# Kernel optimization log

Measured on AMD Instinct MI355X. Metric: run time of the kernel, lower is better.

## Reference

```python
import jax, jax.numpy as jnp
import numpy as np

N = 100000
E = 1600000
D_IN = 128
H = 128
C = 3
EPS_BN = 1e-5
EPS_LN = 1e-5


def _gcn_conv(x, W, b, src, dst, ew, n):
    # PyG GCNConv: x' = D^{-1/2} (A + I) D^{-1/2} (x W) + b, self-loop weight 1
    x = x @ W
    loop = jnp.arange(n)
    src2 = jnp.concatenate([src, loop])
    dst2 = jnp.concatenate([dst, loop])
    ew2 = jnp.concatenate([ew, jnp.ones((n,), dtype=x.dtype)])
    deg = jax.ops.segment_sum(ew2, dst2, num_segments=n)
    dinv = jnp.where(deg > 0, jax.lax.rsqrt(jnp.maximum(deg, 1e-12)), 0.0)
    norm = dinv[src2] * ew2 * dinv[dst2]  # [E+N]
    msgs = x[src2] * norm[:, None]        # [E+N, H] gathered messages
    out = jax.ops.segment_sum(msgs, dst2, num_segments=n)
    return out + b


def setup_inputs() -> dict:
    key = jax.random.key(0)
    ks = jax.random.split(key, 16)
    def lin(k, i, o):
        s = 1.0 / np.sqrt(i)
        k1, k2 = jax.random.split(k)
        return (jax.random.uniform(k1, (i, o), jnp.float32, -s, s),
                jax.random.uniform(k2, (o,), jnp.float32, -s, s))
    x = jax.random.normal(ks[0], (N, D_IN), jnp.float32)
    edge_index = jax.random.randint(ks[1], (2, E), 0, N, jnp.int64)
    edge_attr = jax.random.uniform(ks[2], (E, 1), jnp.float32)
    W_pre, b_pre = lin(ks[3], D_IN, H)
    W1, b1 = lin(ks[4], H, H)
    W2, b2 = lin(ks[5], H, H)
    Wc1, bc1 = lin(ks[6], H, H)
    Wc2, bc2 = lin(ks[7], H, C)
    return {
        "x": x, "edge_index": edge_index, "edge_attr": edge_attr,
        "W_pre": W_pre, "b_pre": b_pre,
        "bn_gamma": jnp.ones((H,), jnp.float32), "bn_beta": jnp.zeros((H,), jnp.float32),
        "bn_mean": jnp.zeros((H,), jnp.float32), "bn_var": jnp.ones((H,), jnp.float32),
        "W1": W1, "b1": b1, "W2": W2, "b2": b2,
        "Wc1": Wc1, "bc1": bc1,
        "ln_g": jnp.ones((H,), jnp.float32), "ln_b": jnp.zeros((H,), jnp.float32),
        "Wc2": Wc2, "bc2": bc2,
    }


def reference(x, edge_index, edge_attr, W_pre, b_pre, bn_gamma, bn_beta, bn_mean, bn_var,
              W1, b1, W2, b2, Wc1, bc1, ln_g, ln_b, Wc2, bc2):
    src, dst = edge_index[0], edge_index[1]
    ew = edge_attr.squeeze()
    n = x.shape[0]
    # input_preprocess: Linear -> BatchNorm1d (eval: running stats) -> ReLU (dropout=identity)
    h = x @ W_pre + b_pre
    h = (h - bn_mean) * jax.lax.rsqrt(bn_var + EPS_BN) * bn_gamma + bn_beta
    h = jax.nn.relu(h)
    residual = h
    # conv layer 1 (+ ReLU, dropout identity in eval)
    h = jax.nn.relu(_gcn_conv(h, W1, b1, src, dst, ew, n))
    # conv layer 2 (last: no activation)
    h = _gcn_conv(h, W2, b2, src, dst, ew, n)
    h = h + residual  # shapes match
    # classifier: Linear -> LayerNorm -> ReLU -> (dropout) -> Linear
    z = h @ Wc1 + bc1
    mu = jnp.mean(z, axis=-1, keepdims=True)
    var = jnp.mean((z - mu) ** 2, axis=-1, keepdims=True)
    z = (z - mu) * jax.lax.rsqrt(var + EPS_LN) * ln_g + ln_b
    z = jax.nn.relu(z)
    return z @ Wc2 + bc2
```

## Files before the change

kernel.cpp:

```cpp
#include <hip/hip_runtime.h>
#include <hip/hip_bf16.h>

typedef __bf16 bf16_t;
typedef bf16_t bf16x8 __attribute__((ext_vector_type(8)));
typedef bf16_t bf16x4 __attribute__((ext_vector_type(4)));
typedef float f32x4 __attribute__((ext_vector_type(4)));
typedef float f32x2 __attribute__((ext_vector_type(2)));

#define EPS_BN 1e-5f
#define EPS_LN 1e-5f
#define SLOTS 32
#define WSCALE 32767.f
#define WINV (1.f / 32767.f)
#define RNODES 448
#define OV_CAP 16384
#define OVA_CAP 65536

__device__ __forceinline__ float blo(unsigned u) { return __uint_as_float(u << 16); }
__device__ __forceinline__ float bhi(unsigned u) { return __uint_as_float(u & 0xFFFF0000u); }
__device__ __forceinline__ f32x2 f8lo(unsigned u) { return __builtin_amdgcn_cvt_pk_f32_fp8((int)u, false); }
__device__ __forceinline__ f32x2 f8hi(unsigned u) { return __builtin_amdgcn_cvt_pk_f32_fp8((int)u, true); }


__global__ void prepK(const float* __restrict__ W0, const float* __restrict__ W1,
                      const float* __restrict__ W2, const float* __restrict__ W3,
                      bf16_t* __restrict__ WT, int* __restrict__ bCnt,
                      int* __restrict__ ovCnt, int* __restrict__ ovACnt) {
    int flat = blockIdx.x * 256 + threadIdx.x;
    if (flat == 0) { *ovCnt = 0; *ovACnt = 0; }
    if (flat < 4096) bCnt[flat] = 0;
    if (flat < 65536) {
        int which = flat >> 14, r = flat & 16383;
        const float* W = (which == 0) ? W0 : (which == 1) ? W1 : (which == 2) ? W2 : W3;
        int i = r >> 7, o = r & 127;
        WT[which * 128 * 136 + o * 136 + i] = (bf16_t)W[r];
    }
}


__global__ __launch_bounds__(256) void binK(
    const int* __restrict__ ei, const float* __restrict__ ea,
    uint2* __restrict__ bbuf, int* __restrict__ bCnt,
    uint2* __restrict__ ovA, int* __restrict__ ovACnt,
    int E, int cap, int nbuck)
{
    __shared__ int lcnt[256];
    __shared__ int gbase[256];
    int tid = threadIdx.x;
    if (tid < nbuck) lcnt[tid] = 0;
    __syncthreads();

    int e0 = blockIdx.x * 4096 + tid;
    int d[16]; unsigned pk[16]; int p[16];
#pragma unroll
    for (int k = 0; k < 16; ++k) {
        int e = e0 + k * 256;
        p[k] = -1;
        if (e < E) {
            d[k] = ei[E + e];
            int s = ei[e];
            unsigned wq = __float2uint_rn(ea[e] * WSCALE);
            pk[k] = ((unsigned)s << 15) | wq;
            p[k] = atomicAdd(&lcnt[(unsigned)d[k] / RNODES], 1);
        }
    }
    __syncthreads();
    if (tid < nbuck) gbase[tid] = atomicAdd(&bCnt[tid * 16], lcnt[tid]);
    __syncthreads();
#pragma unroll
    for (int k = 0; k < 16; ++k) {
        if (p[k] >= 0) {
            int b = (unsigned)d[k] / RNODES;
            int idx = gbase[b] + p[k];
            if (idx < cap) {
                bbuf[(size_t)b * cap + idx] = make_uint2((unsigned)d[k], pk[k]);
            } else {
                int o = atomicAdd(ovACnt, 1);
                if (o < OVA_CAP) ovA[o] = make_uint2((unsigned)d[k], pk[k]);
            }
        }
    }
}


__global__ __launch_bounds__(256) void buildK(
    const uint2* __restrict__ bbuf, const int* __restrict__ bCnt,
    const uint2* __restrict__ ovA, const int* __restrict__ ovACnt,
    unsigned* __restrict__ slots, int* __restrict__ cnt, float* __restrict__ dinv,
    uint2* __restrict__ ov, int* __restrict__ ovCnt,
    int cap, int n)
{
    __shared__ unsigned slotsL[RNODES * 32];
    __shared__ int cntL[RNODES];
    __shared__ float wsumL[RNODES];
    int tid = threadIdx.x;
    int base = blockIdx.x * RNODES;

    for (int j = tid; j < RNODES; j += 256) { cntL[j] = 0; wsumL[j] = 0.f; }
    __syncthreads();

    int nb = min(bCnt[blockIdx.x * 16], cap);
    const uint2* buf = bbuf + (size_t)blockIdx.x * cap;
    for (int i = tid; i < nb; i += 256) {
        uint2 u = buf[i];
        int local = (int)u.x - base;
        int pos = atomicAdd(&cntL[local], 1);
        atomicAdd(&wsumL[local], (float)(u.y & 32767u) * WINV);
        if (pos < SLOTS) {
            slotsL[local * 32 + pos] = u.y;
        } else {
            int o = atomicAdd(ovCnt, 1);
            if (o < OV_CAP) ov[o] = u;
        }
    }
    int no = min(*ovACnt, OVA_CAP);
    for (int k = tid; k < no; k += 256) {
        uint2 u = ovA[k];
        int local = (int)u.x - base;
        if (local >= 0 && local < RNODES) {
            int pos = atomicAdd(&cntL[local], 1);
            atomicAdd(&wsumL[local], (float)(u.y & 32767u) * WINV);
            if (pos < SLOTS) {
                slotsL[local * 32 + pos] = u.y;
            } else {
                int o = atomicAdd(ovCnt, 1);
                if (o < OV_CAP) ov[o] = u;
            }
        }
    }
    __syncthreads();

    for (int j = tid; j < RNODES; j += 256) {
        int node = base + j;
        if (node < n) {
            int c = cntL[j];
            int cm = min(c, SLOTS);
            int c8 = (cm + 7) & ~7;
            for (int k2 = cm; k2 < c8; ++k2) slotsL[j * 32 + k2] = (unsigned)node << 15;
            cnt[node] = c;
            dinv[node] = rsqrtf(fmaxf(1.f + wsumL[j], 1e-12f));
        }
    }
    __syncthreads();

    int vnodes = min(n - base, RNODES);
    if (vnodes <= 0) return;
    const uint4* sl4 = (const uint4*)slotsL;
    uint4* sg4 = (uint4*)(slots + ((size_t)base << 5));
    int lim = vnodes * 8;
    for (int i = tid; i < lim; i += 256) sg4[i] = sl4[i];
}


template <int MODE, typename AT>
__global__ __launch_bounds__(256) void gemm128K(
    const AT* __restrict__ A, const bf16_t* __restrict__ WT,
    bf16_t* __restrict__ outb, unsigned* __restrict__ out8,
    const float* __restrict__ colBias,
    const float* __restrict__ bnMean, const float* __restrict__ bnVar,
    const float* __restrict__ bnG, const float* __restrict__ bnB,
    const float* __restrict__ dinv, int nrows, int ngroups)
{
    __shared__ __align__(16) bf16_t Bs[128 * 136];
    int tid = threadIdx.x;

    {
        const uint4* src = (const uint4*)WT;
        uint4* dst = (uint4*)Bs;
        if (MODE == 1) {
            for (int i = tid; i < 128 * 17; i += 256) {
                int row = i / 17, k = i - row * 17;
                int so = ((row & 15) << 3) | (row >> 4);
                dst[row * 17 + k] = src[so * 17 + k];
            }
        } else {
            for (int i = tid; i < 128 * 17; i += 256) dst[i] = src[i];
        }
    }

    int lane = tid & 63;
    int wid = tid >> 6;
    int m = lane & 15, q = lane >> 4;

    float cb[8], scale[8], shift[8];
    if (MODE == 0) {
#pragma unroll
        for (int c = 0; c < 8; ++c) {
            int j = c * 16 + m;
            cb[c] = colBias[j];
            float rs = rsqrtf(bnVar[j] + EPS_BN);
            scale[c] = bnG[j] * rs;
            shift[c] = bnB[j] - bnMean[j] * scale[c];
        }
    }

    __syncthreads();

    for (int g = blockIdx.x; g < ngroups; g += gridDim.x) {
        int rb = g * 64;
        int myRow = rb + wid * 16 + m;
        int rowL = min(myRow, nrows - 1);

        bf16x8 af[4];
        if constexpr (sizeof(AT) == 4) {
#pragma unroll
            for (int kk = 0; kk < 4; ++kk) {
                float4 v0 = ((const float4*)A)[rowL * 32 + q * 2 + kk * 8];
                float4 v1 = ((const float4*)A)[rowL * 32 + q * 2 + kk * 8 + 1];
                bf16x8 w8;
                w8[0] = (bf16_t)v0.x; w8[1] = (bf16_t)v0.y; w8[2] = (bf16_t)v0.z; w8[3] = (bf16_t)v0.w;
                w8[4] = (bf16_t)v1.x; w8[5] = (bf16_t)v1.y; w8[6] = (bf16_t)v1.z; w8[7] = (bf16_t)v1.w;
                af[kk] = w8;
            }
        } else {
#pragma unroll
            for (int kk = 0; kk < 4; ++kk)
                af[kk] = ((const bf16x8*)A)[rowL * 16 + q + kk * 4];
        }

        f32x4 acc[8];
#pragma unroll
        for (int c = 0; c < 8; ++c) acc[c] = (f32x4){0.f, 0.f, 0.f, 0.f};

#pragma unroll
        for (int kk = 0; kk < 4; ++kk) {
#pragma unroll
            for (int c = 0; c < 8; ++c) {
                bf16x8 bfr = *(const bf16x8*)&Bs[(c * 16 + m) * 136 + q * 8 + kk * 32];
                acc[c] = __builtin_amdgcn_mfma_f32_16x16x32_bf16(af[kk], bfr, acc[c], 0, 0, 0);
            }
        }

        int r0 = rb + wid * 16 + q * 4;
        if (MODE == 1) {
            float dv[4];
#pragma unroll
            for (int i = 0; i < 4; ++i) dv[i] = (r0 + i < nrows) ? dinv[r0 + i] : 0.f;
#pragma unroll
            for (int i = 0; i < 4; ++i) {
                int r = r0 + i;
                if (r < nrows) {
                    float v0 = acc[0][i] * dv[i], v1 = acc[1][i] * dv[i];
                    float v2 = acc[2][i] * dv[i], v3 = acc[3][i] * dv[i];
                    float v4 = acc[4][i] * dv[i], v5 = acc[5][i] * dv[i];
                    float v6 = acc[6][i] * dv[i], v7 = acc[7][i] * dv[i];
                    int lo = __builtin_amdgcn_cvt_pk_fp8_f32(v0, v1, 0, false);
                    lo = __builtin_amdgcn_cvt_pk_fp8_f32(v2, v3, lo, true);
                    int hi = __builtin_amdgcn_cvt_pk_fp8_f32(v4, v5, 0, false);
                    hi = __builtin_amdgcn_cvt_pk_fp8_f32(v6, v7, hi, true);
                    ((uint2*)out8)[(r << 4) | m] = make_uint2((unsigned)lo, (unsigned)hi);
                }
            }
        } else {
#pragma unroll
            for (int c = 0; c < 8; ++c) {
#pragma unroll
                for (int i = 0; i < 4; ++i) {
                    int r = r0 + i;
                    if (r < nrows) {
                        float v = (acc[c][i] + cb[c]) * scale[c] + shift[c];
                        outb[r * 128 + (c * 16 + m)] = (bf16_t)fmaxf(v, 0.f);
                    }
                }
            }
        }
    }
}


#define ACC8(U, W) do { \
    f32x2 Wv = (f32x2){(W), (W)}; \
    acc[0] += Wv * f8lo((U).x); acc[1] += Wv * f8hi((U).x); \
    acc[2] += Wv * f8lo((U).y); acc[3] += Wv * f8hi((U).y); \
    acc[4] += Wv * f8lo((U).z); acc[5] += Wv * f8hi((U).z); \
    acc[6] += Wv * f8lo((U).w); acc[7] += Wv * f8hi((U).w); } while (0)

template <int RELU, int RES>
__global__ __launch_bounds__(256) void aggK(
    const uint4* __restrict__ ts16, const unsigned* __restrict__ slots,
    const int* __restrict__ cnt, const float* __restrict__ dinv,
    const float4* __restrict__ bias, const uint4* __restrict__ residual,
    uint4* __restrict__ out,
    const uint2* __restrict__ ov, const int* __restrict__ ovCnt, int n)
{
    int tid = threadIdx.x;
    int node = blockIdx.x * 8 + (tid >> 5);
    int hl = tid & 31;
    int hb = tid & 32;
    if (node >= n) return;
    int slot = hl >> 3;
    int f = hl & 7;

    int c8 = (min(cnt[node], SLOTS) + 7) & ~7;
    int nit = c8 >> 3;
    unsigned my = slots[(node << 5) | hl];
    float myw = (float)(my & 32767u) * WINV;
    int myoff = (int)(my >> 15) << 3;

    uint4 su = ts16[(node << 3) + f];

    int s0 = hb + slot;
    int po0 = __shfl(myoff, s0);
    int po1 = __shfl(myoff, s0 + 4);
    float pw0 = __shfl(myw, s0);
    float pw1 = __shfl(myw, s0 + 4);
    uint4 u0 = su, u1 = su;
    if (nit > 0) { u0 = ts16[po0 + f]; u1 = ts16[po1 + f]; }

    f32x2 acc[8];
#pragma unroll
    for (int k = 0; k < 8; ++k) acc[k] = (f32x2){0.f, 0.f};

    if (slot == 1) {
        acc[0] += f8lo(su.x); acc[1] += f8hi(su.x);
        acc[2] += f8lo(su.y); acc[3] += f8hi(su.y);
        acc[4] += f8lo(su.z); acc[5] += f8hi(su.z);
        acc[6] += f8lo(su.w); acc[7] += f8hi(su.w);
    }

    for (int j = 0; j < nit; ++j) {
        uint4 v0 = u0, v1 = u1;
        float x0 = pw0, x1 = pw1;
        if (j + 1 < nit) {
            int s = hb + (j + 1) * 8 + slot;
            int no0 = __shfl(myoff, s);
            int no1 = __shfl(myoff, s + 4);
            pw0 = __shfl(myw, s);
            pw1 = __shfl(myw, s + 4);
            u0 = ts16[no0 + f];
            u1 = ts16[no1 + f];
        }
        ACC8(v0, x0);
        ACC8(v1, x1);
    }

    int no = min(*ovCnt, OV_CAP);
    for (int k = 0; k < no; ++k) {
        uint2 ovk = ov[k];
        if ((int)ovk.x == node && slot == 0) {
            uint4 uo = ts16[((int)(ovk.y >> 15) << 3) + f];
            float wo = (float)(ovk.y & 32767u) * WINV;
            ACC8(uo, wo);
        }
    }

#pragma unroll
    for (int k = 0; k < 8; ++k) {
        f32x2 t;
        t.x = __shfl_xor(acc[k].x, 8);  t.y = __shfl_xor(acc[k].y, 8);
        acc[k] += t;
        t.x = __shfl_xor(acc[k].x, 16); t.y = __shfl_xor(acc[k].y, 16);
        acc[k] += t;
    }

    if (slot == 0) {
        float di = dinv[node];
        float r[16];
#pragma unroll
        for (int k = 0; k < 8; ++k) {
            float4 bb = bias[f * 4 + (k >> 1)];
            float b0 = (k & 1) ? bb.z : bb.x;
            float b1 = (k & 1) ? bb.w : bb.y;
            r[2 * k]     = acc[k].x * di + b0;
            r[2 * k + 1] = acc[k].y * di + b1;
        }
        if (RES) {
            uint4 q0 = residual[(node << 4) + f * 2];
            uint4 q1 = residual[(node << 4) + f * 2 + 1];
            r[0] += blo(q0.x);  r[1] += bhi(q0.x);
            r[2] += blo(q0.y);  r[3] += bhi(q0.y);
            r[4] += blo(q0.z);  r[5] += bhi(q0.z);
            r[6] += blo(q0.w);  r[7] += bhi(q0.w);
            r[8] += blo(q1.x);  r[9] += bhi(q1.x);
            r[10] += blo(q1.y); r[11] += bhi(q1.y);
            r[12] += blo(q1.z); r[13] += bhi(q1.z);
            r[14] += blo(q1.w); r[15] += bhi(q1.w);
        }
        if (RELU) {
#pragma unroll
            for (int k = 0; k < 16; ++k) r[k] = fmaxf(r[k], 0.f);
        }
        bf16x8 o0, o1;
#pragma unroll
        for (int k = 0; k < 8; ++k) { o0[k] = (bf16_t)r[k]; o1[k] = (bf16_t)r[8 + k]; }
        out[(node << 4) + f * 2]     = *(uint4*)&o0;
        out[(node << 4) + f * 2 + 1] = *(uint4*)&o1;
    }
}


__global__ __launch_bounds__(256) void classifierK(
    const bf16_t* __restrict__ A, const bf16_t* __restrict__ WT,
    const float* __restrict__ bc1, const float* __restrict__ g,
    const float* __restrict__ b, const float* __restrict__ Wc2,
    const float* __restrict__ bc2, float* __restrict__ out, int nrows, int ngroups)
{
    __shared__ __align__(16) bf16_t Bs[128 * 136];
    __shared__ float sB[128], sG[128], sLb[128], sW2[384];
    int tid = threadIdx.x;

    {
        const uint4* src = (const uint4*)WT;
        uint4* dst = (uint4*)Bs;
        for (int i = tid; i < 128 * 17; i += 256) dst[i] = src[i];
    }
    if (tid < 128) { sB[tid] = bc1[tid]; sG[tid] = g[tid]; sLb[tid] = b[tid]; }
    for (int i = tid; i < 384; i += 256) sW2[i] = Wc2[i];

    int lane = tid & 63;
    int wid = tid >> 6;
    int m = lane & 15, q = lane >> 4;

    __syncthreads();

    for (int grp = blockIdx.x; grp < ngroups; grp += gridDim.x) {
        int rb = grp * 64;
        int rowL = min(rb + wid * 16 + m, nrows - 1);

        bf16x8 af[4];
#pragma unroll
        for (int kk = 0; kk < 4; ++kk)
            af[kk] = ((const bf16x8*)A)[rowL * 16 + q + kk * 4];

        f32x4 acc[8];
#pragma unroll
        for (int c = 0; c < 8; ++c) acc[c] = (f32x4){0.f, 0.f, 0.f, 0.f};
#pragma unroll
        for (int kk = 0; kk < 4; ++kk) {
#pragma unroll
            for (int c = 0; c < 8; ++c) {
                bf16x8 bfr = *(const bf16x8*)&Bs[(c * 16 + m) * 136 + q * 8 + kk * 32];
                acc[c] = __builtin_amdgcn_mfma_f32_16x16x32_bf16(af[kk], bfr, acc[c], 0, 0, 0);
            }
        }

        int r0 = rb + wid * 16 + q * 4;
#pragma unroll
        for (int i = 0; i < 4; ++i) {
            float s1 = 0.f, s2 = 0.f;
#pragma unroll
            for (int c = 0; c < 8; ++c) {
                float z = acc[c][i] + sB[c * 16 + m];
                acc[c][i] = z;
                s1 += z; s2 += z * z;
            }
#pragma unroll
            for (int off = 1; off < 16; off <<= 1) {
                s1 += __shfl_xor(s1, off);
                s2 += __shfl_xor(s2, off);
            }
            float mu = s1 * (1.f / 128.f);
            float var = s2 * (1.f / 128.f) - mu * mu;
            float rstd = rsqrtf(var + EPS_LN);
            float p0 = 0.f, p1 = 0.f, p2 = 0.f;
#pragma unroll
            for (int c = 0; c < 8; ++c) {
                int j = c * 16 + m;
                float zn = (acc[c][i] - mu) * rstd * sG[j] + sLb[j];
                zn = fmaxf(zn, 0.f);
                p0 += zn * sW2[j * 3 + 0];
                p1 += zn * sW2[j * 3 + 1];
                p2 += zn * sW2[j * 3 + 2];
            }
#pragma unroll
            for (int off = 1; off < 16; off <<= 1) {
                p0 += __shfl_xor(p0, off);
                p1 += __shfl_xor(p1, off);
                p2 += __shfl_xor(p2, off);
            }
            int r = r0 + i;
            if (m == 0 && r < nrows) {
                out[r * 3 + 0] = p0 + bc2[0];
                out[r * 3 + 1] = p1 + bc2[1];
                out[r * 3 + 2] = p2 + bc2[2];
            }
        }
    }
}


extern "C" void kernel_launch(void* const* d_in, const int* in_sizes, int n_in,
                              void* d_out, int out_size, void* d_ws, size_t ws_size,
                              hipStream_t stream) {
    const float* x      = (const float*)d_in[0];
    const int*   ei     = (const int*)d_in[1];
    const float* ea     = (const float*)d_in[2];
    const float* W_pre  = (const float*)d_in[3];
    const float* b_pre  = (const float*)d_in[4];
    const float* bn_g   = (const float*)d_in[5];
    const float* bn_b   = (const float*)d_in[6];
    const float* bn_m   = (const float*)d_in[7];
    const float* bn_v   = (const float*)d_in[8];
    const float* W1     = (const float*)d_in[9];
    const float* b1     = (const float*)d_in[10];
    const float* W2     = (const float*)d_in[11];
    const float* b2     = (const float*)d_in[12];
    const float* Wc1    = (const float*)d_in[13];
    const float* bc1    = (const float*)d_in[14];
    const float* ln_g   = (const float*)d_in[15];
    const float* ln_b   = (const float*)d_in[16];
    const float* Wc2    = (const float*)d_in[17];
    const float* bc2    = (const float*)d_in[18];
    float* outp = (float*)d_out;

    const int N = in_sizes[0] / 128;
    const int E = in_sizes[2];

    char* p = (char*)d_ws;
    auto alloc = [&](size_t bytes) -> void* {
        void* r = (void*)p;
        p += (bytes + 255) & ~(size_t)255;
        return r;
    };
    bf16_t*   h0    = (bf16_t*)alloc((size_t)N * 128 * 2);
    bf16_t*   bufB  = (bf16_t*)alloc((size_t)N * 128 * 2);
    unsigned* ts8   = (unsigned*)alloc((size_t)N * 128);
    float*    dinv  = (float*)alloc((size_t)N * 4);
    int*      cnt   = (int*)alloc((size_t)N * 4);
    int*      ovCnt = (int*)alloc(256);
    int*      ovACnt= (int*)alloc(256);
    uint2*    ov    = (uint2*)alloc((size_t)OV_CAP * 8);
    uint2*    ovA   = (uint2*)alloc((size_t)OVA_CAP * 8);
    unsigned* slots = (unsigned*)alloc((size_t)N * SLOTS * 4);
    bf16_t*   WT    = (bf16_t*)alloc((size_t)4 * 128 * 136 * 2);
    int       nbuck = (N + RNODES - 1) / RNODES;
    int       cap   = E / nbuck + 4096;
    uint2*    bbuf  = (uint2*)alloc((size_t)nbuck * cap * 8);
    int*      bCnt  = (int*)alloc(4096 * 4);

    bf16_t* WT_pre = WT + 0 * 128 * 136;
    bf16_t* WT_1   = WT + 1 * 128 * 136;
    bf16_t* WT_2   = WT + 2 * 128 * 136;
    bf16_t* WT_c1  = WT + 3 * 128 * 136;

    int gG = (N + 63) / 64;
    int nBlk = gG < 1024 ? gG : 1024;
    int gH = (N + 7) / 8;
    int gP = 65536 / 256;
    int gBin = (E + 4095) / 4096;

    prepK<<<gP, 256, 0, stream>>>(W_pre, W1, W2, Wc1, WT, bCnt, ovCnt, ovACnt);
    binK<<<gBin, 256, 0, stream>>>(ei, ea, bbuf, bCnt, ovA, ovACnt, E, cap, nbuck);
    buildK<<<nbuck, 256, 0, stream>>>(bbuf, bCnt, ovA, ovACnt, slots, cnt, dinv, ov, ovCnt, cap, N);

    gemm128K<0, float><<<nBlk, 256, 0, stream>>>(x, WT_pre, h0, nullptr, b_pre, bn_m, bn_v, bn_g, bn_b, nullptr, N, gG);
    gemm128K<1, bf16_t><<<nBlk, 256, 0, stream>>>(h0, WT_1, nullptr, ts8, nullptr, nullptr, nullptr, nullptr, nullptr, dinv, N, gG);
    aggK<1, 0><<<gH, 256, 0, stream>>>((const uint4*)ts8, slots, cnt, dinv, (const float4*)b1,
                                       nullptr, (uint4*)bufB, ov, ovCnt, N);
    gemm128K<1, bf16_t><<<nBlk, 256, 0, stream>>>(bufB, WT_2, nullptr, ts8, nullptr, nullptr, nullptr, nullptr, nullptr, dinv, N, gG);
    aggK<0, 1><<<gH, 256, 0, stream>>>((const uint4*)ts8, slots, cnt, dinv, (const float4*)b2,
                                       (const uint4*)h0, (uint4*)bufB, ov, ovCnt, N);
    classifierK<<<nBlk, 256, 0, stream>>>(bufB, WT_c1, bc1, ln_g, ln_b, Wc2, bc2, outp, N, gG);
}
```

Before: 341.1 us.

## Fuse GEMMs with neighbor aggregation into three per-tile kernels through shared memory

Replaces the six-kernel chain (pre-GEMM, W1 GEMM, aggregate, W2 GEMM, aggregate, classifier) with three 512-thread kernels. Each kernel handles a 128-row tile, runs the aggregation or first GEMM into a shared-memory tile, restages the next weight matrix into the same buffer, and runs the following GEMM from LDS. This removes the bf16 intermediate round trips through global memory and cuts launch count. In exchange the aggregation loses its software prefetch of the next gather, processes 8 nodes sequentially per half-wave, and the grid shrinks to N/128 blocks with heavy LDS use, which may limit latency hiding for the gathers.

```diff
diff --git a/kernel.cpp b/kernel.cpp
--- a/kernel.cpp
+++ b/kernel.cpp
@@ -3,7 +3,6 @@
 
 typedef __bf16 bf16_t;
 typedef bf16_t bf16x8 __attribute__((ext_vector_type(8)));
-typedef bf16_t bf16x4 __attribute__((ext_vector_type(4)));
 typedef float f32x4 __attribute__((ext_vector_type(4)));
 typedef float f32x2 __attribute__((ext_vector_type(2)));
 
@@ -20,6 +19,13 @@
 __device__ __forceinline__ float bhi(unsigned u) { return __uint_as_float(u & 0xFFFF0000u); }
 __device__ __forceinline__ f32x2 f8lo(unsigned u) { return __builtin_amdgcn_cvt_pk_f32_fp8((int)u, false); }
 __device__ __forceinline__ f32x2 f8hi(unsigned u) { return __builtin_amdgcn_cvt_pk_f32_fp8((int)u, true); }
+
+#define ACC8(U, W) do { \
+    f32x2 Wv = (f32x2){(W), (W)}; \
+    acc[0] += Wv * f8lo((U).x); acc[1] += Wv * f8hi((U).x); \
+    acc[2] += Wv * f8lo((U).y); acc[3] += Wv * f8hi((U).y); \
+    acc[4] += Wv * f8lo((U).z); acc[5] += Wv * f8hi((U).z); \
+    acc[6] += Wv * f8lo((U).w); acc[7] += Wv * f8hi((U).w); } while (0)
 
 
 __global__ void prepK(const float* __restrict__ W0, const float* __restrict__ W1,
@@ -152,328 +158,358 @@
 }
 
 
-template <int MODE, typename AT>
-__global__ __launch_bounds__(256) void gemm128K(
-    const AT* __restrict__ A, const bf16_t* __restrict__ WT,
-    bf16_t* __restrict__ outb, unsigned* __restrict__ out8,
-    const float* __restrict__ colBias,
-    const float* __restrict__ bnMean, const float* __restrict__ bnVar,
-    const float* __restrict__ bnG, const float* __restrict__ bnB,
-    const float* __restrict__ dinv, int nrows, int ngroups)
-{
-    __shared__ __align__(16) bf16_t Bs[128 * 136];
-    int tid = threadIdx.x;
-
-    {
-        const uint4* src = (const uint4*)WT;
-        uint4* dst = (uint4*)Bs;
-        if (MODE == 1) {
-            for (int i = tid; i < 128 * 17; i += 256) {
-                int row = i / 17, k = i - row * 17;
-                int so = ((row & 15) << 3) | (row >> 4);
-                dst[row * 17 + k] = src[so * 17 + k];
-            }
-        } else {
-            for (int i = tid; i < 128 * 17; i += 256) dst[i] = src[i];
-        }
-    }
-
-    int lane = tid & 63;
-    int wid = tid >> 6;
-    int m = lane & 15, q = lane >> 4;
-
-    float cb[8], scale[8], shift[8];
-    if (MODE == 0) {
-#pragma unroll
-        for (int c = 0; c < 8; ++c) {
-            int j = c * 16 + m;
-            cb[c] = colBias[j];
-            float rs = rsqrtf(bnVar[j] + EPS_BN);
-            scale[c] = bnG[j] * rs;
-            shift[c] = bnB[j] - bnMean[j] * scale[c];
-        }
-    }
-
-    __syncthreads();
-
-    for (int g = blockIdx.x; g < ngroups; g += gridDim.x) {
-        int rb = g * 64;
-        int myRow = rb + wid * 16 + m;
-        int rowL = min(myRow, nrows - 1);
-
-        bf16x8 af[4];
-        if constexpr (sizeof(AT) == 4) {
-#pragma unroll
-            for (int kk = 0; kk < 4; ++kk) {
-                float4 v0 = ((const float4*)A)[rowL * 32 + q * 2 + kk * 8];
-                float4 v1 = ((const float4*)A)[rowL * 32 + q * 2 + kk * 8 + 1];
-                bf16x8 w8;
-                w8[0] = (bf16_t)v0.x; w8[1] = (bf16_t)v0.y; w8[2] = (bf16_t)v0.z; w8[3] = (bf16_t)v0.w;
-                w8[4] = (bf16_t)v1.x; w8[5] = (bf16_t)v1.y; w8[6] = (bf16_t)v1.z; w8[7] = (bf16_t)v1.w;
-                af[kk] = w8;
-            }
-        } else {
-#pragma unroll
-            for (int kk = 0; kk < 4; ++kk)
-                af[kk] = ((const bf16x8*)A)[rowL * 16 + q + kk * 4];
-        }
-
-        f32x4 acc[8];
-#pragma unroll
-        for (int c = 0; c < 8; ++c) acc[c] = (f32x4){0.f, 0.f, 0.f, 0.f};
-
-#pragma unroll
-        for (int kk = 0; kk < 4; ++kk) {
-#pragma unroll
-            for (int c = 0; c < 8; ++c) {
-                bf16x8 bfr = *(const bf16x8*)&Bs[(c * 16 + m) * 136 + q * 8 + kk * 32];
-                acc[c] = __builtin_amdgcn_mfma_f32_16x16x32_bf16(af[kk], bfr, acc[c], 0, 0, 0);
-            }
-        }
-
-        int r0 = rb + wid * 16 + q * 4;
-        if (MODE == 1) {
-            float dv[4];
-#pragma unroll
-            for (int i = 0; i < 4; ++i) dv[i] = (r0 + i < nrows) ? dinv[r0 + i] : 0.f;
-#pragma unroll
-            for (int i = 0; i < 4; ++i) {
-                int r = r0 + i;
-                if (r < nrows) {
-                    float v0 = acc[0][i] * dv[i], v1 = acc[1][i] * dv[i];
-                    float v2 = acc[2][i] * dv[i], v3 = acc[3][i] * dv[i];
-                    float v4 = acc[4][i] * dv[i], v5 = acc[5][i] * dv[i];
-                    float v6 = acc[6][i] * dv[i], v7 = acc[7][i] * dv[i];
-                    int lo = __builtin_amdgcn_cvt_pk_fp8_f32(v0, v1, 0, false);
-                    lo = __builtin_amdgcn_cvt_pk_fp8_f32(v2, v3, lo, true);
-                    int hi = __builtin_amdgcn_cvt_pk_fp8_f32(v4, v5, 0, false);
-                    hi = __builtin_amdgcn_cvt_pk_fp8_f32(v6, v7, hi, true);
-                    ((uint2*)out8)[(r << 4) | m] = make_uint2((unsigned)lo, (unsigned)hi);
-                }
-            }
-        } else {
-#pragma unroll
-            for (int c = 0; c < 8; ++c) {
-#pragma unroll
-                for (int i = 0; i < 4; ++i) {
-                    int r = r0 + i;
-                    if (r < nrows) {
-                        float v = (acc[c][i] + cb[c]) * scale[c] + shift[c];
-                        outb[r * 128 + (c * 16 + m)] = (bf16_t)fmaxf(v, 0.f);
-                    }
-                }
-            }
-        }
-    }
-}
-
-
-#define ACC8(U, W) do { \
-    f32x2 Wv = (f32x2){(W), (W)}; \
-    acc[0] += Wv * f8lo((U).x); acc[1] += Wv * f8hi((U).x); \
-    acc[2] += Wv * f8lo((U).y); acc[3] += Wv * f8hi((U).y); \
-    acc[4] += Wv * f8lo((U).z); acc[5] += Wv * f8hi((U).z); \
-    acc[6] += Wv * f8lo((U).w); acc[7] += Wv * f8hi((U).w); } while (0)
+__device__ __forceinline__ void stageB(const bf16_t* __restrict__ WT, bf16_t* __restrict__ Bs,
+                                       int tid, bool perm) {
+    const uint4* src = (const uint4*)WT;
+    uint4* dst = (uint4*)Bs;
+    if (perm) {
+        for (int i = tid; i < 128 * 17; i += 512) {
+            int row = i / 17, k = i - row * 17;
+            int so = ((row & 15) << 3) | (row >> 4);
+            dst[row * 17 + k] = src[so * 17 + k];
+        }
+    } else {
+        for (int i = tid; i < 128 * 17; i += 512) dst[i] = src[i];
+    }
+}
 
 template <int RELU, int RES>
-__global__ __launch_bounds__(256) void aggK(
+__device__ __forceinline__ void aggPhase(
+    int rb, int n, int tid,
     const uint4* __restrict__ ts16, const unsigned* __restrict__ slots,
     const int* __restrict__ cnt, const float* __restrict__ dinv,
     const float4* __restrict__ bias, const uint4* __restrict__ residual,
-    uint4* __restrict__ out,
+    const uint2* __restrict__ ov, const int* __restrict__ ovCnt,
+    bf16_t* __restrict__ hT)
+{
+    int hw = tid >> 5;
+    int hl = tid & 31;
+    int hb = tid & 32;
+    int slot = hl >> 3;
+    int f = hl & 7;
+    int no = min(*ovCnt, OV_CAP);
+
+    for (int p = 0; p < 8; ++p) {
+        int node = rb + hw + 16 * p;
+        if (node >= n) break;
+
+        int c8 = (min(cnt[node], SLOTS) + 7) & ~7;
+        unsigned my = slots[(node << 5) | hl];
+        float myw = (float)(my & 32767u) * WINV;
+        int myoff = (int)(my >> 15) << 3;
+
+        f32x2 acc[8];
+#pragma unroll
+        for (int k = 0; k < 8; ++k) acc[k] = (f32x2){0.f, 0.f};
+
+        uint4 su = ts16[(node << 3) + f];
+        if (slot == 1) {
+            acc[0] += f8lo(su.x); acc[1] += f8hi(su.x);
+            acc[2] += f8lo(su.y); acc[3] += f8hi(su.y);
+            acc[4] += f8lo(su.z); acc[5] += f8hi(su.z);
+            acc[6] += f8lo(su.w); acc[7] += f8hi(su.w);
+        }
+
+        for (int j = 0; j < c8; j += 8) {
+            int s0 = hb + j + slot;
+            int s1 = s0 + 4;
+            int o0 = __shfl(myoff, s0);
+            int o1 = __shfl(myoff, s1);
+            float w0 = __shfl(myw, s0);
+            float w1 = __shfl(myw, s1);
+            uint4 u0 = ts16[o0 + f];
+            uint4 u1 = ts16[o1 + f];
+            ACC8(u0, w0);
+            ACC8(u1, w1);
+        }
+
+        for (int k = 0; k < no; ++k) {
+            uint2 ovk = ov[k];
+            if ((int)ovk.x == node && slot == 0) {
+                uint4 uo = ts16[((int)(ovk.y >> 15) << 3) + f];
+                float wo = (float)(ovk.y & 32767u) * WINV;
+                ACC8(uo, wo);
+            }
+        }
+
+#pragma unroll
+        for (int k = 0; k < 8; ++k) {
+            f32x2 t;
+            t.x = __shfl_xor(acc[k].x, 8);  t.y = __shfl_xor(acc[k].y, 8);
+            acc[k] += t;
+            t.x = __shfl_xor(acc[k].x, 16); t.y = __shfl_xor(acc[k].y, 16);
+            acc[k] += t;
+        }
+
+        if (slot == 0) {
+            float di = dinv[node];
+            float r[16];
+#pragma unroll
+            for (int k = 0; k < 8; ++k) {
+                float4 bb = bias[f * 4 + (k >> 1)];
+                float b0 = (k & 1) ? bb.z : bb.x;
+                float b1 = (k & 1) ? bb.w : bb.y;
+                r[2 * k]     = acc[k].x * di + b0;
+                r[2 * k + 1] = acc[k].y * di + b1;
+            }
+            if (RES) {
+                uint4 q0 = residual[(node << 4) + f * 2];
+                uint4 q1 = residual[(node << 4) + f * 2 + 1];
+                r[0] += blo(q0.x);  r[1] += bhi(q0.x);
+                r[2] += blo(q0.y);  r[3] += bhi(q0.y);
+                r[4] += blo(q0.z);  r[5] += bhi(q0.z);
+                r[6] += blo(q0.w);  r[7] += bhi(q0.w);
+                r[8] += blo(q1.x);  r[9] += bhi(q1.x);
+                r[10] += blo(q1.y); r[11] += bhi(q1.y);
+                r[12] += blo(q1.z); r[13] += bhi(q1.z);
+                r[14] += blo(q1.w); r[15] += bhi(q1.w);
+            }
+            if (RELU) {
+#pragma unroll
+                for (int k = 0; k < 16; ++k) r[k] = fmaxf(r[k], 0.f);
+            }
+            bf16x8 o0, o1;
+#pragma unroll
+            for (int k = 0; k < 8; ++k) { o0[k] = (bf16_t)r[k]; o1[k] = (bf16_t)r[8 + k]; }
+            uint4* dst = (uint4*)&hT[(node - rb) * 136 + f * 16];
+            dst[0] = *(uint4*)&o0;
+            dst[1] = *(uint4*)&o1;
+        }
+    }
+}
+
+__device__ __forceinline__ void mfma128(const bf16_t* __restrict__ Bs, const bf16x8* af,
+                                        f32x4* acc, int m, int q) {
+#pragma unroll
+    for (int kk = 0; kk < 4; ++kk) {
+#pragma unroll
+        for (int c = 0; c < 8; ++c) {
+            bf16x8 bfr = *(const bf16x8*)&Bs[(c * 16 + m) * 136 + q * 8 + kk * 32];
+            acc[c] = __builtin_amdgcn_mfma_f32_16x16x32_bf16(af[kk], bfr, acc[c], 0, 0, 0);
+        }
+    }
+}
+
+
+__global__ __launch_bounds__(512) void fusePreK(
+    const float* __restrict__ x, const bf16_t* __restrict__ WTpre, const bf16_t* __restrict__ WT1,
+    bf16_t* __restrict__ h0, unsigned* __restrict__ ts8,
+    const float* __restrict__ b_pre,
+    const float* __restrict__ bnMean, const float* __restrict__ bnVar,
+    const float* __restrict__ bnG, const float* __restrict__ bnB,
+    const float* __restrict__ dinv, int n)
+{
+    __shared__ __align__(16) bf16_t U[128 * 136];
+    int tid = threadIdx.x;
+    int rb = blockIdx.x * 128;
+    int lane = tid & 63, wid = tid >> 6;
+    int m = lane & 15, q = lane >> 4;
+
+    stageB(WTpre, U, tid, true);
+
+    float scale[8], shift[8];
+#pragma unroll
+    for (int c = 0; c < 8; ++c) {
+        int j = m * 8 + c;
+        float rs = rsqrtf(bnVar[j] + EPS_BN);
+        scale[c] = bnG[j] * rs;
+        shift[c] = bnB[j] - bnMean[j] * scale[c] + b_pre[j] * scale[c];
+    }
+
+    int rowL = min(rb + wid * 16 + m, n - 1);
+    bf16x8 af[4];
+#pragma unroll
+    for (int kk = 0; kk < 4; ++kk) {
+        float4 v0 = ((const float4*)x)[rowL * 32 + q * 2 + kk * 8];
+        float4 v1 = ((const float4*)x)[rowL * 32 + q * 2 + kk * 8 + 1];
+        bf16x8 w8;
+        w8[0] = (bf16_t)v0.x; w8[1] = (bf16_t)v0.y; w8[2] = (bf16_t)v0.z; w8[3] = (bf16_t)v0.w;
+        w8[4] = (bf16_t)v1.x; w8[5] = (bf16_t)v1.y; w8[6] = (bf16_t)v1.z; w8[7] = (bf16_t)v1.w;
+        af[kk] = w8;
+    }
+    __syncthreads();
+
+    f32x4 acc[8];
+#pragma unroll
+    for (int c = 0; c < 8; ++c) acc[c] = (f32x4){0.f, 0.f, 0.f, 0.f};
+    mfma128(U, af, acc, m, q);
+    __syncthreads();
+
+    int r0 = rb + wid * 16 + q * 4;
+#pragma unroll
+    for (int i = 0; i < 4; ++i) {
+        bf16x8 hv;
+#pragma unroll
+        for (int c = 0; c < 8; ++c)
+            hv[c] = (bf16_t)fmaxf(acc[c][i] * scale[c] + shift[c], 0.f);
+        int lr = wid * 16 + q * 4 + i;
+        *(uint4*)&U[lr * 136 + m * 8] = *(uint4*)&hv;
+        int r = r0 + i;
+        if (r < n) ((uint4*)h0)[r * 16 + m] = *(uint4*)&hv;
+    }
+    __syncthreads();
+
+    int lrow = min(wid * 16 + m, 127);
+#pragma unroll
+    for (int kk = 0; kk < 4; ++kk)
+        af[kk] = *(const bf16x8*)&U[lrow * 136 + q * 8 + kk * 32];
+    __syncthreads();
+    stageB(WT1, U, tid, true);
+    __syncthreads();
+
+#pragma unroll
+    for (int c = 0; c < 8; ++c) acc[c] = (f32x4){0.f, 0.f, 0.f, 0.f};
+    mfma128(U, af, acc, m, q);
+
+    float dv[4];
+#pragma unroll
+    for (int i = 0; i < 4; ++i) dv[i] = (r0 + i < n) ? dinv[r0 + i] : 0.f;
+#pragma unroll
+    for (int i = 0; i < 4; ++i) {
+        int r = r0 + i;
+        if (r < n) {
+            float v0 = acc[0][i] * dv[i], v1 = acc[1][i] * dv[i];
+            float v2 = acc[2][i] * dv[i], v3 = acc[3][i] * dv[i];
+            float v4 = acc[4][i] * dv[i], v5 = acc[5][i] * dv[i];
+            float v6 = acc[6][i] * dv[i], v7 = acc[7][i] * dv[i];
+            int lo = __builtin_amdgcn_cvt_pk_fp8_f32(v0, v1, 0, false);
+            lo = __builtin_amdgcn_cvt_pk_fp8_f32(v2, v3, lo, true);
+            int hi = __builtin_amdgcn_cvt_pk_fp8_f32(v4, v5, 0, false);
+            hi = __builtin_amdgcn_cvt_pk_fp8_f32(v6, v7, hi, true);
+            ((uint2*)ts8)[(r << 4) | m] = make_uint2((unsigned)lo, (unsigned)hi);
+        }
+    }
+}
+
+
+__global__ __launch_bounds__(512) void fuseConvK(
+    const uint4* __restrict__ ts16, const unsigned* __restrict__ slots,
+    const int* __restrict__ cnt, const float* __restrict__ dinv,
+    const float4* __restrict__ bias, const bf16_t* __restrict__ WT2,
+    unsigned* __restrict__ out8,
     const uint2* __restrict__ ov, const int* __restrict__ ovCnt, int n)
 {
+    __shared__ __align__(16) bf16_t U[128 * 136];
     int tid = threadIdx.x;
-    int node = blockIdx.x * 8 + (tid >> 5);
-    int hl = tid & 31;
-    int hb = tid & 32;
-    if (node >= n) return;
-    int slot = hl >> 3;
-    int f = hl & 7;
-
-    int c8 = (min(cnt[node], SLOTS) + 7) & ~7;
-    int nit = c8 >> 3;
-    unsigned my = slots[(node << 5) | hl];
-    float myw = (float)(my & 32767u) * WINV;
-    int myoff = (int)(my >> 15) << 3;
-
-    uint4 su = ts16[(node << 3) + f];
-
-    int s0 = hb + slot;
-    int po0 = __shfl(myoff, s0);
-    int po1 = __shfl(myoff, s0 + 4);
-    float pw0 = __shfl(myw, s0);
-    float pw1 = __shfl(myw, s0 + 4);
-    uint4 u0 = su, u1 = su;
-    if (nit > 0) { u0 = ts16[po0 + f]; u1 = ts16[po1 + f]; }
-
-    f32x2 acc[8];
-#pragma unroll
-    for (int k = 0; k < 8; ++k) acc[k] = (f32x2){0.f, 0.f};
-
-    if (slot == 1) {
-        acc[0] += f8lo(su.x); acc[1] += f8hi(su.x);
-        acc[2] += f8lo(su.y); acc[3] += f8hi(su.y);
-        acc[4] += f8lo(su.z); acc[5] += f8hi(su.z);
-        acc[6] += f8lo(su.w); acc[7] += f8hi(su.w);
-    }
-
-    for (int j = 0; j < nit; ++j) {
-        uint4 v0 = u0, v1 = u1;
-        float x0 = pw0, x1 = pw1;
-        if (j + 1 < nit) {
-            int s = hb + (j + 1) * 8 + slot;
-            int no0 = __shfl(myoff, s);
-            int no1 = __shfl(myoff, s + 4);
-            pw0 = __shfl(myw, s);
-            pw1 = __shfl(myw, s + 4);
-            u0 = ts16[no0 + f];
-            u1 = ts16[no1 + f];
-        }
-        ACC8(v0, x0);
-        ACC8(v1, x1);
-    }
-
-    int no = min(*ovCnt, OV_CAP);
-    for (int k = 0; k < no; ++k) {
-        uint2 ovk = ov[k];
-        if ((int)ovk.x == node && slot == 0) {
-            uint4 uo = ts16[((int)(ovk.y >> 15) << 3) + f];
-            float wo = (float)(ovk.y & 32767u) * WINV;
-            ACC8(uo, wo);
-        }
-    }
-
-#pragma unroll
-    for (int k = 0; k < 8; ++k) {
-        f32x2 t;
-        t.x = __shfl_xor(acc[k].x, 8);  t.y = __shfl_xor(acc[k].y, 8);
-        acc[k] += t;
-        t.x = __shfl_xor(acc[k].x, 16); t.y = __shfl_xor(acc[k].y, 16);
-        acc[k] += t;
-    }
-
-    if (slot == 0) {
-        float di = dinv[node];
-        float r[16];
-#pragma unroll
-        for (int k = 0; k < 8; ++k) {
-            float4 bb = bias[f * 4 + (k >> 1)];
-            float b0 = (k & 1) ? bb.z : bb.x;
-            float b1 = (k & 1) ? bb.w : bb.y;
-            r[2 * k]     = acc[k].x * di + b0;
-            r[2 * k + 1] = acc[k].y * di + b1;
-        }
-        if (RES) {
-            uint4 q0 = residual[(node << 4) + f * 2];
-            uint4 q1 = residual[(node << 4) + f * 2 + 1];
-            r[0] += blo(q0.x);  r[1] += bhi(q0.x);
-            r[2] += blo(q0.y);  r[3] += bhi(q0.y);
-            r[4] += blo(q0.z);  r[5] += bhi(q0.z);
-            r[6] += blo(q0.w);  r[7] += bhi(q0.w);
-            r[8] += blo(q1.x);  r[9] += bhi(q1.x);
-            r[10] += blo(q1.y); r[11] += bhi(q1.y);
-            r[12] += blo(q1.z); r[13] += bhi(q1.z);
-            r[14] += blo(q1.w); r[15] += bhi(q1.w);
-        }
-        if (RELU) {
-#pragma unroll
-            for (int k = 0; k < 16; ++k) r[k] = fmaxf(r[k], 0.f);
-        }
-        bf16x8 o0, o1;
-#pragma unroll
-        for (int k = 0; k < 8; ++k) { o0[k] = (bf16_t)r[k]; o1[k] = (bf16_t)r[8 + k]; }
-        out[(node << 4) + f * 2]     = *(uint4*)&o0;
-        out[(node << 4) + f * 2 + 1] = *(uint4*)&o1;
-    }
-}
-
-
-__global__ __launch_bounds__(256) void classifierK(
-    const bf16_t* __restrict__ A, const bf16_t* __restrict__ WT,
+    int rb = blockIdx.x * 128;
+
+    aggPhase<1, 0>(rb, n, tid, ts16, slots, cnt, dinv, bias, nullptr, ov, ovCnt, U);
+    __syncthreads();
+
+    int lane = tid & 63, wid = tid >> 6;
+    int m = lane & 15, q = lane >> 4;
+    int lrow = min(wid * 16 + m, max(n - 1 - rb, 0));
+    bf16x8 af[4];
+#pragma unroll
+    for (int kk = 0; kk < 4; ++kk)
+        af[kk] = *(const bf16x8*)&U[lrow * 136 + q * 8 + kk * 32];
+    __syncthreads();
+    stageB(WT2, U, tid, true);
+    __syncthreads();
+
+    f32x4 acc[8];
+#pragma unroll
+    for (int c = 0; c < 8; ++c) acc[c] = (f32x4){0.f, 0.f, 0.f, 0.f};
+    mfma128(U, af, acc, m, q);
+
+    int r0 = rb + wid * 16 + q * 4;
+    float dv[4];
+#pragma unroll
+    for (int i = 0; i < 4; ++i) dv[i] = (r0 + i < n) ? dinv[r0 + i] : 0.f;
+#pragma unroll
+    for (int i = 0; i < 4; ++i) {
+        int r = r0 + i;
+        if (r < n) {
+            float v0 = acc[0][i] * dv[i], v1 = acc[1][i] * dv[i];
+            float v2 = acc[2][i] * dv[i], v3 = acc[3][i] * dv[i];
+            float v4 = acc[4][i] * dv[i], v5 = acc[5][i] * dv[i];
+            float v6 = acc[6][i] * dv[i], v7 = acc[7][i] * dv[i];
+            int lo = __builtin_amdgcn_cvt_pk_fp8_f32(v0, v1, 0, false);
+            lo = __builtin_amdgcn_cvt_pk_fp8_f32(v2, v3, lo, true);
+            int hi = __builtin_amdgcn_cvt_pk_fp8_f32(v4, v5, 0, false);
+            hi = __builtin_amdgcn_cvt_pk_fp8_f32(v6, v7, hi, true);
+            ((uint2*)out8)[(r << 4) | m] = make_uint2((unsigned)lo, (unsigned)hi);
+        }
+    }
+}
+
+
+__global__ __launch_bounds__(512) void fuseClsK(
+    const uint4* __restrict__ ts16, const unsigned* __restrict__ slots,
+    const int* __restrict__ cnt, const float* __restrict__ dinv,
+    const float4* __restrict__ bias, const uint4* __restrict__ residual,
+    const bf16_t* __restrict__ WTc1,
     const float* __restrict__ bc1, const float* __restrict__ g,
     const float* __restrict__ b, const float* __restrict__ Wc2,
-    const float* __restrict__ bc2, float* __restrict__ out, int nrows, int ngroups)
+    const float* __restrict__ bc2, float* __restrict__ out,
+    const uint2* __restrict__ ov, const int* __restrict__ ovCnt, int n)
 {
-    __shared__ __align__(16) bf16_t Bs[128 * 136];
+    __shared__ __align__(16) bf16_t U[128 * 136];
     __shared__ float sB[128], sG[128], sLb[128], sW2[384];
     int tid = threadIdx.x;
-
-    {
-        const uint4* src = (const uint4*)WT;
-        uint4* dst = (uint4*)Bs;
-        for (int i = tid; i < 128 * 17; i += 256) dst[i] = src[i];
-    }
+    int rb = blockIdx.x * 128;
+
     if (tid < 128) { sB[tid] = bc1[tid]; sG[tid] = g[tid]; sLb[tid] = b[tid]; }
-    for (int i = tid; i < 384; i += 256) sW2[i] = Wc2[i];
-
-    int lane = tid & 63;
-    int wid = tid >> 6;
+    else if (tid < 512) { int i = tid - 128; if (i < 384) sW2[i] = Wc2[i]; }
+
+    aggPhase<0, 1>(rb, n, tid, ts16, slots, cnt, dinv, bias, residual, ov, ovCnt, U);
+    __syncthreads();
+
+    int lane = tid & 63, wid = tid >> 6;
     int m = lane & 15, q = lane >> 4;
-
-    __syncthreads();
-
-    for (int grp = blockIdx.x; grp < ngroups; grp += gridDim.x) {
-        int rb = grp * 64;
-        int rowL = min(rb + wid * 16 + m, nrows - 1);
-
-        bf16x8 af[4];
-#pragma unroll
-        for (int kk = 0; kk < 4; ++kk)
-            af[kk] = ((const bf16x8*)A)[rowL * 16 + q + kk * 4];
-
-        f32x4 acc[8];
-#pragma unroll
-        for (int c = 0; c < 8; ++c) acc[c] = (f32x4){0.f, 0.f, 0.f, 0.f};
-#pragma unroll
-        for (int kk = 0; kk < 4; ++kk) {
-#pragma unroll
-            for (int c = 0; c < 8; ++c) {
-                bf16x8 bfr = *(const bf16x8*)&Bs[(c * 16 + m) * 136 + q * 8 + kk * 32];
-                acc[c] = __builtin_amdgcn_mfma_f32_16x16x32_bf16(af[kk], bfr, acc[c], 0, 0, 0);
-            }
-        }
-
-        int r0 = rb + wid * 16 + q * 4;
-#pragma unroll
-        for (int i = 0; i < 4; ++i) {
-            float s1 = 0.f, s2 = 0.f;
-#pragma unroll
-            for (int c = 0; c < 8; ++c) {
-                float z = acc[c][i] + sB[c * 16 + m];
-                acc[c][i] = z;
-                s1 += z; s2 += z * z;
-            }
-#pragma unroll
-            for (int off = 1; off < 16; off <<= 1) {
-                s1 += __shfl_xor(s1, off);
-                s2 += __shfl_xor(s2, off);
-            }
-            float mu = s1 * (1.f / 128.f);
-            float var = s2 * (1.f / 128.f) - mu * mu;
-            float rstd = rsqrtf(var + EPS_LN);
-            float p0 = 0.f, p1 = 0.f, p2 = 0.f;
-#pragma unroll
-            for (int c = 0; c < 8; ++c) {
-                int j = c * 16 + m;
-                float zn = (acc[c][i] - mu) * rstd * sG[j] + sLb[j];
-                zn = fmaxf(zn, 0.f);
-                p0 += zn * sW2[j * 3 + 0];
-                p1 += zn * sW2[j * 3 + 1];
-                p2 += zn * sW2[j * 3 + 2];
-            }
-#pragma unroll
-            for (int off = 1; off < 16; off <<= 1) {
-                p0 += __shfl_xor(p0, off);
-                p1 += __shfl_xor(p1, off);
-                p2 += __shfl_xor(p2, off);
-            }
-            int r = r0 + i;
-            if (m == 0 && r < nrows) {
-                out[r * 3 + 0] = p0 + bc2[0];
-                out[r * 3 + 1] = p1 + bc2[1];
-                out[r * 3 + 2] = p2 + bc2[2];
-            }
+    int lrow = min(wid * 16 + m, max(n - 1 - rb, 0));
+    bf16x8 af[4];
+#pragma unroll
+    for (int kk = 0; kk < 4; ++kk)
+        af[kk] = *(const bf16x8*)&U[lrow * 136 + q * 8 + kk * 32];
+    __syncthreads();
+    stageB(WTc1, U, tid, false);
+    __syncthreads();
+
+    f32x4 acc[8];
+#pragma unroll
+    for (int c = 0; c < 8; ++c) acc[c] = (f32x4){0.f, 0.f, 0.f, 0.f};
+    mfma128(U, af, acc, m, q);
+
+    int r0 = rb + wid * 16 + q * 4;
+#pragma unroll
+    for (int i = 0; i < 4; ++i) {
+        float s1 = 0.f, s2 = 0.f;
+#pragma unroll
+        for (int c = 0; c < 8; ++c) {
+            float z = acc[c][i] + sB[c * 16 + m];
+            acc[c][i] = z;
+            s1 += z; s2 += z * z;
+        }
+#pragma unroll
+        for (int off = 1; off < 16; off <<= 1) {
+            s1 += __shfl_xor(s1, off);
+            s2 += __shfl_xor(s2, off);
+        }
+        float mu = s1 * (1.f / 128.f);
+        float var = s2 * (1.f / 128.f) - mu * mu;
+        float rstd = rsqrtf(var + EPS_LN);
+        float p0 = 0.f, p1 = 0.f, p2 = 0.f;
+#pragma unroll
+        for (int c = 0; c < 8; ++c) {
+            int j = c * 16 + m;
+            float zn = (acc[c][i] - mu) * rstd * sG[j] + sLb[j];
+            zn = fmaxf(zn, 0.f);
+            p0 += zn * sW2[j * 3 + 0];
+            p1 += zn * sW2[j * 3 + 1];
+            p2 += zn * sW2[j * 3 + 2];
+        }
+#pragma unroll
+        for (int off = 1; off < 16; off <<= 1) {
+            p0 += __shfl_xor(p0, off);
+            p1 += __shfl_xor(p1, off);
+            p2 += __shfl_xor(p2, off);
+        }
+        int r = r0 + i;
+        if (m == 0 && r < n) {
+            out[r * 3 + 0] = p0 + bc2[0];
+            out[r * 3 + 1] = p1 + bc2[1];
+            out[r * 3 + 2] = p2 + bc2[2];
         }
     }
 }
@@ -513,8 +549,8 @@
         return r;
     };
     bf16_t*   h0    = (bf16_t*)alloc((size_t)N * 128 * 2);
-    bf16_t*   bufB  = (bf16_t*)alloc((size_t)N * 128 * 2);
     unsigned* ts8   = (unsigned*)alloc((size_t)N * 128);
+    unsigned* ts8b  = (unsigned*)alloc((size_t)N * 128);
     float*    dinv  = (float*)alloc((size_t)N * 4);
     int*      cnt   = (int*)alloc((size_t)N * 4);
     int*      ovCnt = (int*)alloc(256);
@@ -533,9 +569,7 @@
     bf16_t* WT_2   = WT + 2 * 128 * 136;
     bf16_t* WT_c1  = WT + 3 * 128 * 136;
 
-    int gG = (N + 63) / 64;
-    int nBlk = gG < 1024 ? gG : 1024;
-    int gH = (N + 7) / 8;
+    int gF = (N + 127) / 128;
     int gP = 65536 / 256;
     int gBin = (E + 4095) / 4096;
 
@@ -543,12 +577,10 @@
     binK<<<gBin, 256, 0, stream>>>(ei, ea, bbuf, bCnt, ovA, ovACnt, E, cap, nbuck);
     buildK<<<nbuck, 256, 0, stream>>>(bbuf, bCnt, ovA, ovACnt, slots, cnt, dinv, ov, ovCnt, cap, N);
 
-    gemm128K<0, float><<<nBlk, 256, 0, stream>>>(x, WT_pre, h0, nullptr, b_pre, bn_m, bn_v, bn_g, bn_b, nullptr, N, gG);
-    gemm128K<1, bf16_t><<<nBlk, 256, 0, stream>>>(h0, WT_1, nullptr, ts8, nullptr, nullptr, nullptr, nullptr, nullptr, dinv, N, gG);
-    aggK<1, 0><<<gH, 256, 0, stream>>>((const uint4*)ts8, slots, cnt, dinv, (const float4*)b1,
-                                       nullptr, (uint4*)bufB, ov, ovCnt, N);
-    gemm128K<1, bf16_t><<<nBlk, 256, 0, stream>>>(bufB, WT_2, nullptr, ts8, nullptr, nullptr, nullptr, nullptr, nullptr, dinv, N, gG);
-    aggK<0, 1><<<gH, 256, 0, stream>>>((const uint4*)ts8, slots, cnt, dinv, (const float4*)b2,
-                                       (const uint4*)h0, (uint4*)bufB, ov, ovCnt, N);
-    classifierK<<<nBlk, 256, 0, stream>>>(bufB, WT_c1, bc1, ln_g, ln_b, Wc2, bc2, outp, N, gG);
-}
+    fusePreK<<<gF, 512, 0, stream>>>(x, WT_pre, WT_1, h0, ts8, b_pre, bn_m, bn_v, bn_g, bn_b, dinv, N);
+    fuseConvK<<<gF, 512, 0, stream>>>((const uint4*)ts8, slots, cnt, dinv, (const float4*)b1,
+                                      WT_2, ts8b, ov, ovCnt, N);
+    fuseClsK<<<gF, 512, 0, stream>>>((const uint4*)ts8b, slots, cnt, dinv, (const float4*)b2,
+                                     (const uint4*)h0, WT_c1, bc1, ln_g, ln_b, Wc2, bc2, outp,
+                                     ov, ovCnt, N);
+}
```

Measured after the change: 431.4 us. 1.26x slower.
